# Performance work log

Measured on AMD Instinct MI355X. Metric: run time of the kernel, lower is better.

## Reference

```python
import jax, jax.numpy as jnp
import numpy as np

S, B, D, H, V = 1024, 4, 1024, 4096, 32000
EPS = 1e-5

def _ln(x, g, b):
    m = jnp.mean(x, axis=-1, keepdims=True)
    v = jnp.var(x, axis=-1, keepdims=True)
    return (x - m) * jax.lax.rsqrt(v + EPS) * g + b

def setup_inputs() -> dict:
    key = jax.random.key(0)
    ks = jax.random.split(key, 12)
    def xav(k, shape):
        fan_in, fan_out = shape[1], shape[0]
        lim = np.sqrt(6.0 / (fan_in + fan_out))
        return jax.random.uniform(k, shape, jnp.float32, -lim, lim)
    return {
        "inputs": jax.random.randint(ks[0], (S, B), 0, V, dtype=jnp.int32),
        "emb_table": jax.random.normal(ks[1], (V, D), jnp.float32),
        "WQ": xav(ks[2], (D, D)),
        "WK": xav(ks[3], (D, D)),
        "WV": xav(ks[4], (D, D)),
        "Wo": xav(ks[5], (D, D)),
        "bo": jnp.zeros((D,), jnp.float32),
        "W1": xav(ks[6], (H, D)),
        "b1": jnp.zeros((H,), jnp.float32),
        "W2": xav(ks[7], (D, H)),
        "b2": jnp.zeros((D,), jnp.float32),
        "g1": jnp.ones((D,), jnp.float32),
        "be1": jnp.zeros((D,), jnp.float32),
        "g2": jnp.ones((D,), jnp.float32),
        "be2": jnp.zeros((D,), jnp.float32),
        "Wd": xav(ks[8], (V, D)),
        "bd": jnp.zeros((V,), jnp.float32),
    }

def reference(inputs, emb_table, WQ, WK, WV, Wo, bo, W1, b1, W2, b2, g1, be1, g2, be2, Wd, bd):
    # inputs: [S, B] int ids
    emb = emb_table[inputs]                       # [S, B, D]
    # F.linear(x, W) == x @ W.T
    Q = jnp.einsum('sbd,ed->bse', emb, WQ)        # [B, S, D]
    K = jnp.einsum('sbd,ed->bse', emb, WK)
    Vv = jnp.einsum('sbd,ed->bse', emb, WV)
    scores = jnp.einsum('bqd,bkd->bqk', Q, K) / jnp.sqrt(jnp.float32(D))
    attn = jax.nn.softmax(scores, axis=-1)        # [B, S, S]
    z = jnp.einsum('bqk,bkd->qbd', attn, Vv)      # back to [S, B, D]
    z = jnp.einsum('sbd,ed->sbe', z, Wo) + bo
    x = _ln(emb + z, g1, be1)
    ffn = jnp.einsum('sbh,dh->sbd', jax.nn.relu(jnp.einsum('sbd,hd->sbh', x, W1) + b1), W2) + b2
    out = _ln(x + ffn, g2, be2)
    logits = out.reshape(S * B, D) @ Wd.T + bd    # [S*B, V]
    return logits
```

## Files before the change

kernel.cpp:

```cpp
#include <hip/hip_runtime.h>

typedef float f32x4 __attribute__((ext_vector_type(4)));
typedef __bf16 bf16x8 __attribute__((ext_vector_type(8)));
typedef int i32x4 __attribute__((ext_vector_type(4)));
typedef unsigned short u16;
typedef unsigned short u16x4 __attribute__((ext_vector_type(4)));
typedef unsigned short u16x8 __attribute__((ext_vector_type(8)));
typedef unsigned int u32;

#define SEQ 1024
#define NBATCH 4
#define DM 1024
#define HD 4096
#define NV 32000
#define NT (SEQ * NBATCH)

__device__ __forceinline__ u16 f2bf(float f) {
  u32 u = __builtin_bit_cast(u32, f);
  return (u16)((u + 0x7FFFu + ((u >> 16) & 1u)) >> 16);
}

__global__ __launch_bounds__(256) void cast_bf16_kernel(const float* __restrict__ in,
                                                        u16* __restrict__ out, int n8) {
  int i = blockIdx.x * 256 + threadIdx.x;
  if (i >= n8) return;
  const f32x4* p = (const f32x4*)(in + (long)i * 8);
  f32x4 a = p[0], b = p[1];
  u16x8 o;
  o[0] = f2bf(a[0]); o[1] = f2bf(a[1]); o[2] = f2bf(a[2]); o[3] = f2bf(a[3]);
  o[4] = f2bf(b[0]); o[5] = f2bf(b[1]); o[6] = f2bf(b[2]); o[7] = f2bf(b[3]);
  *(u16x8*)(out + (long)i * 8) = o;
}

__global__ __launch_bounds__(256) void embed_kernel(const int* __restrict__ ids,
                                                    const float* __restrict__ tab,
                                                    float* __restrict__ ef,
                                                    u16* __restrict__ eh) {
  int t = blockIdx.x, tid = threadIdx.x;
  long id = ids[t];
  f32x4 v = *(const f32x4*)(tab + id * DM + tid * 4);
  *(f32x4*)(ef + (long)t * DM + tid * 4) = v;
  u16x4 h;
  h[0] = f2bf(v[0]); h[1] = f2bf(v[1]); h[2] = f2bf(v[2]); h[3] = f2bf(v[3]);
  *(u16x4*)(eh + (long)t * DM + tid * 4) = h;
}

__global__ __launch_bounds__(256) void softmax_kernel(const float* __restrict__ s,
                                                      u16* __restrict__ p) {
  int row = blockIdx.x, tid = threadIdx.x;
  const float* rp = s + (long)row * SEQ;
  f32x4 v = *(const f32x4*)(rp + tid * 4);
  float mx = fmaxf(fmaxf(v[0], v[1]), fmaxf(v[2], v[3]));
  for (int o = 32; o; o >>= 1) mx = fmaxf(mx, __shfl_xor(mx, o));
  __shared__ float red[4];
  if ((tid & 63) == 0) red[tid >> 6] = mx;
  __syncthreads();
  mx = fmaxf(fmaxf(red[0], red[1]), fmaxf(red[2], red[3]));
  const float sc = 0.03125f;
  f32x4 e;
  e[0] = expf((v[0] - mx) * sc); e[1] = expf((v[1] - mx) * sc);
  e[2] = expf((v[2] - mx) * sc); e[3] = expf((v[3] - mx) * sc);
  float sm = e[0] + e[1] + e[2] + e[3];
  for (int o = 32; o; o >>= 1) sm += __shfl_xor(sm, o);
  __syncthreads();
  if ((tid & 63) == 0) red[tid >> 6] = sm;
  __syncthreads();
  sm = red[0] + red[1] + red[2] + red[3];
  float inv = 1.0f / sm;
  u16x4 o4;
  o4[0] = f2bf(e[0] * inv); o4[1] = f2bf(e[1] * inv);
  o4[2] = f2bf(e[2] * inv); o4[3] = f2bf(e[3] * inv);
  *(u16x4*)(p + (long)row * SEQ + tid * 4) = o4;
}

__global__ __launch_bounds__(256) void ln_kernel(const float* __restrict__ in,
                                                 const float* __restrict__ g,
                                                 const float* __restrict__ be,
                                                 float* __restrict__ outf,
                                                 u16* __restrict__ outh) {
  int row = blockIdx.x, tid = threadIdx.x;
  f32x4 v = *(const f32x4*)(in + (long)row * DM + tid * 4);
  float s = v[0] + v[1] + v[2] + v[3];
  float q = v[0] * v[0] + v[1] * v[1] + v[2] * v[2] + v[3] * v[3];
  for (int o = 32; o; o >>= 1) { s += __shfl_xor(s, o); q += __shfl_xor(q, o); }
  __shared__ float rs_[4], rq_[4];
  if ((tid & 63) == 0) { rs_[tid >> 6] = s; rq_[tid >> 6] = q; }
  __syncthreads();
  s = rs_[0] + rs_[1] + rs_[2] + rs_[3];
  q = rq_[0] + rq_[1] + rq_[2] + rq_[3];
  float mean = s * (1.0f / DM);
  float var = q * (1.0f / DM) - mean * mean;
  float rstd = rsqrtf(var + 1e-5f);
  f32x4 gg = *(const f32x4*)(g + tid * 4);
  f32x4 bb = *(const f32x4*)(be + tid * 4);
  f32x4 y;
  y[0] = (v[0] - mean) * rstd * gg[0] + bb[0];
  y[1] = (v[1] - mean) * rstd * gg[1] + bb[1];
  y[2] = (v[2] - mean) * rstd * gg[2] + bb[2];
  y[3] = (v[3] - mean) * rstd * gg[3] + bb[3];
  if (outf) *(f32x4*)(outf + (long)row * DM + tid * 4) = y;
  if (outh) {
    u16x4 h;
    h[0] = f2bf(y[0]); h[1] = f2bf(y[1]); h[2] = f2bf(y[2]); h[3] = f2bf(y[3]);
    *(u16x4*)(outh + (long)row * DM + tid * 4) = h;
  }
}

__global__ __launch_bounds__(256) void ln_i8_kernel(const float* __restrict__ in,
                                                    const float* __restrict__ g,
                                                    const float* __restrict__ be,
                                                    char* __restrict__ q8,
                                                    float* __restrict__ scale) {
  int row = blockIdx.x, tid = threadIdx.x;
  f32x4 v = *(const f32x4*)(in + (long)row * DM + tid * 4);
  float s = v[0] + v[1] + v[2] + v[3];
  float q = v[0] * v[0] + v[1] * v[1] + v[2] * v[2] + v[3] * v[3];
  for (int o = 32; o; o >>= 1) { s += __shfl_xor(s, o); q += __shfl_xor(q, o); }
  __shared__ float rs_[4], rq_[4], rm_[4];
  if ((tid & 63) == 0) { rs_[tid >> 6] = s; rq_[tid >> 6] = q; }
  __syncthreads();
  s = rs_[0] + rs_[1] + rs_[2] + rs_[3];
  q = rq_[0] + rq_[1] + rq_[2] + rq_[3];
  float mean = s * (1.0f / DM);
  float var = q * (1.0f / DM) - mean * mean;
  float rstd = rsqrtf(var + 1e-5f);
  f32x4 gg = *(const f32x4*)(g + tid * 4);
  f32x4 bb = *(const f32x4*)(be + tid * 4);
  f32x4 y;
  y[0] = (v[0] - mean) * rstd * gg[0] + bb[0];
  y[1] = (v[1] - mean) * rstd * gg[1] + bb[1];
  y[2] = (v[2] - mean) * rstd * gg[2] + bb[2];
  y[3] = (v[3] - mean) * rstd * gg[3] + bb[3];
  float am = fmaxf(fmaxf(fabsf(y[0]), fabsf(y[1])), fmaxf(fabsf(y[2]), fabsf(y[3])));
  for (int o = 32; o; o >>= 1) am = fmaxf(am, __shfl_xor(am, o));
  __syncthreads();
  if ((tid & 63) == 0) rm_[tid >> 6] = am;
  __syncthreads();
  am = fmaxf(fmaxf(rm_[0], rm_[1]), fmaxf(rm_[2], rm_[3]));
  float inv = (am > 0.f) ? 127.f / am : 0.f;
  int q0 = (int)rintf(y[0] * inv), q1 = (int)rintf(y[1] * inv);
  int q2 = (int)rintf(y[2] * inv), q3 = (int)rintf(y[3] * inv);
  u32 pk = (q0 & 255) | ((q1 & 255) << 8) | ((q2 & 255) << 16) | ((u32)(q3 & 255) << 24);
  *(u32*)(q8 + (size_t)row * DM + tid * 4) = pk;
  if (tid == 0) scale[row] = am * (1.0f / 127.f);
}

__global__ __launch_bounds__(256) void rowq_i8_kernel(const float* __restrict__ in,
                                                      char* __restrict__ q8,
                                                      float* __restrict__ scale) {
  int row = blockIdx.x, tid = threadIdx.x;
  f32x4 v = *(const f32x4*)(in + (size_t)row * DM + tid * 4);
  float am = fmaxf(fmaxf(fabsf(v[0]), fabsf(v[1])), fmaxf(fabsf(v[2]), fabsf(v[3])));
  for (int o = 32; o; o >>= 1) am = fmaxf(am, __shfl_xor(am, o));
  __shared__ float rm_[4];
  if ((tid & 63) == 0) rm_[tid >> 6] = am;
  __syncthreads();
  am = fmaxf(fmaxf(rm_[0], rm_[1]), fmaxf(rm_[2], rm_[3]));
  float inv = (am > 0.f) ? 127.f / am : 0.f;
  int q0 = (int)rintf(v[0] * inv), q1 = (int)rintf(v[1] * inv);
  int q2 = (int)rintf(v[2] * inv), q3 = (int)rintf(v[3] * inv);
  u32 pk = (q0 & 255) | ((q1 & 255) << 8) | ((q2 & 255) << 16) | ((u32)(q3 & 255) << 24);
  *(u32*)(q8 + (size_t)row * DM + tid * 4) = pk;
  if (tid == 0) scale[row] = am * (1.0f / 127.f);
}

#define GLD(gp, lp)                                              \
  __builtin_amdgcn_global_load_lds(                              \
      (__attribute__((address_space(1))) void*)(gp),             \
      (__attribute__((address_space(3))) void*)(lp), 16, 0, 0)

#define BM 128
#define BN 128
#define BK 32

__global__ __launch_bounds__(256) void gemm_bt(
    const u16* __restrict__ A, const u16* __restrict__ B,
    float* __restrict__ Cf, u16* __restrict__ Ch,
    const float* __restrict__ bias, const float* __restrict__ resid,
    int K, int lda, int ldb, int ldc,
    long batA, long batB, long batC, int relu) {
  __shared__ u16 As[BM * BK];
  __shared__ u16 Bs[BN * BK];
  const int tid = threadIdx.x;
  const int bz = blockIdx.z;
  A += (long)bz * batA;
  B += (long)bz * batB;
  const long cbase = (long)bz * batC;
  const int row0 = blockIdx.y * BM;
  const int col0 = blockIdx.x * BN;
  const int l = tid & 63;
  const int w = tid >> 6;
  const int wr = (w >> 1) * 64, wc = (w & 1) * 64;

  f32x4 acc[4][4] = {};

  const u16* gA = A + (long)(row0 + (tid >> 2)) * lda + (tid & 3) * 8;
  const u16* gB = B + (long)(col0 + (tid >> 2)) * ldb + (tid & 3) * 8;
  const long a64 = (long)64 * lda, b64 = (long)64 * ldb;
  u16* lA = As + tid * 8;
  u16* lB = Bs + tid * 8;

  const int fr = l & 15;
  const int fk = (l >> 4) * 8;
  const u16* rA = As + (wr + fr) * BK + fk;
  const u16* rB = Bs + (wc + fr) * BK + fk;

  for (int k0 = 0; k0 < K; k0 += BK) {
    GLD(gA + k0, lA);
    GLD(gA + a64 + k0, lA + 2048);
    GLD(gB + k0, lB);
    GLD(gB + b64 + k0, lB + 2048);
    __syncthreads();
    bf16x8 af[4], bf[4];
#pragma unroll
    for (int m = 0; m < 4; ++m) af[m] = *(const bf16x8*)(rA + m * 16 * BK);
#pragma unroll
    for (int n = 0; n < 4; ++n) bf[n] = *(const bf16x8*)(rB + n * 16 * BK);
#pragma unroll
    for (int m = 0; m < 4; ++m)
#pragma unroll
      for (int n = 0; n < 4; ++n)
        acc[m][n] = __builtin_amdgcn_mfma_f32_16x16x32_bf16(af[m], bf[n], acc[m][n], 0, 0, 0);
    __syncthreads();
  }

  const int er = row0 + wr + ((l >> 4) << 2);
  const int ec = col0 + wc + (l & 15);
#pragma unroll
  for (int m = 0; m < 4; ++m) {
#pragma unroll
    for (int n = 0; n < 4; ++n) {
      f32x4 v = acc[m][n];
      const int c = ec + n * 16;
      float bv = bias ? bias[c] : 0.0f;
#pragma unroll
      for (int i = 0; i < 4; ++i) {
        const int r = er + m * 16 + i;
        float x = v[i] + bv;
        if (resid) x += resid[(long)r * ldc + c];
        if (relu) x = fmaxf(x, 0.0f);
        if (Cf) Cf[cbase + (long)r * ldc + c] = x;
        if (Ch) Ch[cbase + (long)r * ldc + c] = f2bf(x);
      }
    }
  }
}

#define DSB() __builtin_amdgcn_sched_barrier(0)
#define SBAR() __builtin_amdgcn_s_barrier()

__global__ __launch_bounds__(256) void gemm_i8(
    const char* __restrict__ A, const char* __restrict__ B,
    float* __restrict__ C, const float* __restrict__ sA, const float* __restrict__ sB,
    const float* __restrict__ bias, int K, int lda, int ldb, int ldc,
    int Mtiles, int Ntiles) {
  __shared__ __align__(16) char As[3][128 * 64];
  __shared__ __align__(16) char Bs[3][128 * 64];
  const int tid = threadIdx.x;

  const int nwg = gridDim.x;
  const int blk = blockIdx.x;
  const int cpx = nwg >> 3;
  const int wg = (blk & 7) * cpx + (blk >> 3);
  const int gsz = 4 * Ntiles;
  const int gid = wg / gsz;
  const int rem = wg - gid * gsz;
  const int row0 = (gid * 4 + (rem & 3)) * 128;
  const int col0 = (rem >> 2) * 128;

  const int l = tid & 63;
  const int w = tid >> 6;
  const int wr = (w >> 1) * 64, wc = (w & 1) * 64;

  const int srow = tid >> 2;
  const int sslot = (tid & 3) ^ ((srow >> 1) & 3);
  const char* gA = A + (size_t)(row0 + srow) * lda + sslot * 16;
  const char* gB = B + (size_t)(col0 + srow) * ldb + sslot * 16;
  const size_t a64 = (size_t)64 * lda, b64 = (size_t)64 * ldb;

#define STAGE_I8(buf, kt)                                            \
  do {                                                               \
    const char* _ga = gA + (size_t)(kt) * 64;                        \
    const char* _gb = gB + (size_t)(kt) * 64;                        \
    GLD(_ga, &As[buf][0] + tid * 16);                                \
    GLD(_ga + a64, &As[buf][4096] + tid * 16);                       \
    GLD(_gb, &Bs[buf][0] + tid * 16);                                \
    GLD(_gb + b64, &Bs[buf][4096] + tid * 16);                       \
  } while (0)

  const int fr = l & 15;
  const int fsw = 16 * ((l >> 4) ^ ((fr >> 1) & 3));
  const int raoff = (wr + fr) * 64 + fsw;
  const int rboff = (wc + fr) * 64 + fsw;

  i32x4 acc[4][4] = {};

#define COMPUTE_I8(buf)                                                         \
  do {                                                                          \
    i32x4 af[4], bf[4];                                                         \
    _Pragma("unroll")                                                           \
    for (int m = 0; m < 4; ++m) af[m] = *(const i32x4*)(&As[buf][raoff + m * 1024]); \
    _Pragma("unroll")                                                           \
    for (int n = 0; n < 4; ++n) bf[n] = *(const i32x4*)(&Bs[buf][rboff + n * 1024]); \
    _Pragma("unroll")                                                           \
    for (int m = 0; m < 4; ++m)                                                 \
      _Pragma("unroll")                                                         \
      for (int n = 0; n < 4; ++n)                                               \
        acc[m][n] = __builtin_amdgcn_mfma_i32_16x16x64_i8(af[m], bf[n], acc[m][n], 0, 0, 0); \
  } while (0)

  const int nkt = K >> 6;

  STAGE_I8(0, 0);
  STAGE_I8(1, 1);
  asm volatile("s_waitcnt vmcnt(4)"); DSB();
  SBAR();

  for (int t = 0; t < nkt - 2; ++t) {
    const int b2 = (t + 2) % 3;
    STAGE_I8(b2, t + 2);
    COMPUTE_I8(t % 3);
    asm volatile("s_waitcnt vmcnt(4)"); DSB();
    SBAR();
  }
  COMPUTE_I8((nkt - 2) % 3);
  asm volatile("s_waitcnt vmcnt(0)"); DSB();
  SBAR();
  COMPUTE_I8((nkt - 1) % 3);

  const int er = row0 + wr + ((l >> 4) << 2);
  const int ec = col0 + wc + (l & 15);
#pragma unroll
  for (int m = 0; m < 4; ++m) {
#pragma unroll
    for (int n = 0; n < 4; ++n) {
      i32x4 v = acc[m][n];
      const int c = ec + n * 16;
      const float sb = sB[c];
      const float bv = bias ? bias[c] : 0.0f;
#pragma unroll
      for (int i = 0; i < 4; ++i) {
        const int r = er + m * 16 + i;
        C[(size_t)r * ldc + c] = (float)v[i] * (sA[r] * sb) + bv;
      }
    }
  }
#undef STAGE_I8
#undef COMPUTE_I8
}

template <int N0, int N1>
__device__ __forceinline__ void mfma16(f32x4 (&acc)[8][4], const bf16x8 (&af)[8],
                                       bf16x8 b0, bf16x8 b1) {
#pragma unroll
  for (int m = 0; m < 8; ++m) {
    acc[m][N0] = __builtin_amdgcn_mfma_f32_16x16x32_bf16(af[m], b0, acc[m][N0], 0, 0, 0);
    acc[m][N1] = __builtin_amdgcn_mfma_f32_16x16x32_bf16(af[m], b1, acc[m][N1], 0, 0, 0);
  }
}

__global__ __launch_bounds__(512, 2) void gemm256_bt(
    const u16* __restrict__ A, const u16* __restrict__ B,
    float* __restrict__ Cf, u16* __restrict__ Ch,
    const float* __restrict__ bias,
    int K, int lda, int ldb, int ldc, int Mtiles, int Ntiles, int relu) {
  __shared__ __align__(16) u16 As[2][2][128 * 64];
  __shared__ __align__(16) u16 Bs[2][2][256 * 32];
  const int tid = threadIdx.x;

  const int nwg = gridDim.x;
  const int blk = blockIdx.x;
  const int cpx = nwg >> 3;
  const int wg = (blk & 7) * cpx + (blk >> 3);
  const int gsz = 4 * Ntiles;
  const int gid = wg / gsz;
  const int rem = wg - gid * gsz;
  const int row0 = (gid * 4 + (rem & 3)) * 256;
  const int col0 = (rem >> 2) * 256;

  const int l = tid & 63;
  const int w = tid >> 6;
  const int wr = w >> 2;
  const int wc = w & 3;

  const int sArow = tid >> 3;
  const int sAcol = ((tid & 7) ^ ((sArow >> 1) & 7)) * 8;
  const int sBrow = tid >> 2;
  const int sBcol = ((tid & 3) ^ ((sBrow >> 2) & 3)) * 8;

  const u16* gA = A + (size_t)(row0 + sArow) * lda + sAcol;
  const u16* gB = B + (size_t)(col0 + sBrow) * ldb + sBcol;
  const size_t a64 = (size_t)64 * lda;
  const size_t b128 = (size_t)128 * ldb;

#define STAGE_A(buf, h, kt)                                          \
  do {                                                               \
    const u16* _g = gA + (size_t)(h) * 128 * lda + (size_t)(kt) * 64;\
    u16* _l = &As[buf][h][0] + tid * 8;                              \
    GLD(_g, _l);                                                     \
    GLD(_g + a64, _l + 4096);                                        \
  } while (0)
#define STAGE_B(buf, kk, kt)                                         \
  do {                                                               \
    const u16* _g = gB + (size_t)(kt) * 64 + (kk) * 32;              \
    u16* _l = &Bs[buf][kk][0] + tid * 8;                             \
    GLD(_g, _l);                                                     \
    GLD(_g + b128, _l + 4096);                                       \
  } while (0)

  const int fr = l & 15;
  const int g8 = (l >> 4) * 8;
  const int acp0 = g8 ^ (((fr >> 1) & 7) * 8);
  const int acp1 = (32 + g8) ^ (((fr >> 1) & 7) * 8);
  const int bcp = g8 ^ (((fr >> 2) & 3) * 8);

#define RA(buf, m, cp) (*(const bf16x8*)(&As[buf][wr][((m) * 16 + fr) * 64 + (cp)]))
#define RB(buf, n, kk) (*(const bf16x8*)(&Bs[buf][kk][(wc * 64 + (n) * 16 + fr) * 32 + bcp]))

  f32x4 acc[8][4] = {};
  bf16x8 a0[8], a1[8], bb0, bb1;

  const int nkt = K >> 6;
  const int nit = nkt >> 1;

  STAGE_A(0, 0, 0); STAGE_A(0, 1, 0);
  STAGE_B(0, 0, 0); STAGE_B(0, 1, 0);
  STAGE_B(1, 0, 1); STAGE_A(1, 0, 1);
  asm volatile("s_waitcnt vmcnt(4)"); DSB();
  SBAR();

  for (int i = 0; i < nit; ++i) {
    const int u = 2 * i + 1;
    const int v = (2 * i + 2 < nkt) ? 2 * i + 2 : nkt - 1;
    const int w2 = (2 * i + 3 < nkt) ? 2 * i + 3 : nkt - 1;

#pragma unroll
    for (int m = 0; m < 8; ++m) a0[m] = RA(0, m, acp0);
    bb0 = RB(0, 0, 0); bb1 = RB(0, 1, 0);
    STAGE_A(1, 1, u);
    SBAR();
    asm volatile("s_waitcnt lgkmcnt(0)"); DSB();
    __builtin_amdgcn_s_setprio(1);
    mfma16<0, 1>(acc, a0, bb0, bb1);
    __builtin_amdgcn_s_setprio(0);
    SBAR();
    bb0 = RB(0, 2, 0); bb1 = RB(0, 3, 0);
    STAGE_B(1, 1, u);
    asm volatile("s_waitcnt vmcnt(6)"); DSB();
    SBAR();
    asm volatile("s_waitcnt lgkmcnt(0)"); DSB();
    __builtin_amdgcn_s_setprio(1);
    mfma16<2, 3>(acc, a0, bb0, bb1);
    __builtin_amdgcn_s_setprio(0);
    SBAR();
#pragma unroll
    for (int m = 0; m < 8; ++m) a1[m] = RA(0, m, acp1);
    bb0 = RB(0, 0, 1); bb1 = RB(0, 1, 1);
    STAGE_B(0, 0, v);
    SBAR();
    asm volatile("s_waitcnt lgkmcnt(0)"); DSB();
    __builtin_amdgcn_s_setprio(1);
    mfma16<0, 1>(acc, a1, bb0, bb1);
    __builtin_amdgcn_s_setprio(0);
    SBAR();
    bb0 = RB(0, 2, 1); bb1 = RB(0, 3, 1);
    STAGE_A(0, 0, v);
    asm volatile("s_waitcnt vmcnt(6)"); DSB();
    SBAR();
    asm volatile("s_waitcnt lgkmcnt(0)"); DSB();
    __builtin_amdgcn_s_setprio(1);
    mfma16<2, 3>(acc, a1, bb0, bb1);
    __builtin_amdgcn_s_setprio(0);
    SBAR();
#pragma unroll
    for (int m = 0; m < 8; ++m) a0[m] = RA(1, m, acp0);
    bb0 = RB(1, 0, 0); bb1 = RB(1, 1, 0);
    STAGE_A(0, 1, v);
    SBAR();
    asm volatile("s_waitcnt lgkmcnt(0)"); DSB();
    __builtin_amdgcn_s_setprio(1);
    mfma16<0, 1>(acc, a0, bb0, bb1);
    __builtin_amdgcn_s_setprio(0);
    SBAR();
    bb0 = RB(1, 2, 0); bb1 = RB(1, 3, 0);
    STAGE_B(0, 1, v);
    asm volatile("s_waitcnt vmcnt(6)"); DSB();
    SBAR();
    asm volatile("s_waitcnt lgkmcnt(0)"); DSB();
    __builtin_amdgcn_s_setprio(1);
    mfma16<2, 3>(acc, a0, bb0, bb1);
    __builtin_amdgcn_s_setprio(0);
    SBAR();
#pragma unroll
    for (int m = 0; m < 8; ++m) a1[m] = RA(1, m, acp1);
    bb0 = RB(1, 0, 1); bb1 = RB(1, 1, 1);
    STAGE_B(1, 0, w2);
    SBAR();
    asm volatile("s_waitcnt lgkmcnt(0)"); DSB();
    __builtin_amdgcn_s_setprio(1);
    mfma16<0, 1>(acc, a1, bb0, bb1);
    __builtin_amdgcn_s_setprio(0);
    SBAR();
    bb0 = RB(1, 2, 1); bb1 = RB(1, 3, 1);
    STAGE_A(1, 0, w2);
    asm volatile("s_waitcnt vmcnt(6)"); DSB();
    SBAR();
    asm volatile("s_waitcnt lgkmcnt(0)"); DSB();
    __builtin_amdgcn_s_setprio(1);
    mfma16<2, 3>(acc, a1, bb0, bb1);
    __builtin_amdgcn_s_setprio(0);
    SBAR();
  }

  asm volatile("s_waitcnt vmcnt(0)"); DSB();

  const int er = row0 + wr * 128 + ((l >> 4) << 2);
  const int ec = col0 + wc * 64 + (l & 15);
#pragma unroll
  for (int m = 0; m < 8; ++m) {
#pragma unroll
    for (int n = 0; n < 4; ++n) {
      f32x4 vv = acc[m][n];
      const int c = ec + n * 16;
      float bv = bias ? bias[c] : 0.0f;
#pragma unroll
      for (int i = 0; i < 4; ++i) {
        const int r = er + m * 16 + i;
        float x = vv[i] + bv;
        if (relu) x = fmaxf(x, 0.0f);
        if (Cf) Cf[(size_t)r * ldc + c] = x;
        if (Ch) Ch[(size_t)r * ldc + c] = f2bf(x);
      }
    }
  }
#undef STAGE_A
#undef STAGE_B
#undef RA
#undef RB
}

extern "C" void kernel_launch(void* const* d_in, const int* in_sizes, int n_in,
                              void* d_out, int out_size, void* d_ws, size_t ws_size,
                              hipStream_t stream) {
  const int* ids = (const int*)d_in[0];
  const float* tab = (const float*)d_in[1];
  const float* WQ = (const float*)d_in[2];
  const float* WK = (const float*)d_in[3];
  const float* WV = (const float*)d_in[4];
  const float* Wo = (const float*)d_in[5];
  const float* bo = (const float*)d_in[6];
  const float* W1 = (const float*)d_in[7];
  const float* b1 = (const float*)d_in[8];
  const float* W2 = (const float*)d_in[9];
  const float* b2 = (const float*)d_in[10];
  const float* g1 = (const float*)d_in[11];
  const float* be1 = (const float*)d_in[12];
  const float* g2 = (const float*)d_in[13];
  const float* be2 = (const float*)d_in[14];
  const float* Wd = (const float*)d_in[15];
  const float* bd = (const float*)d_in[16];
  float* logits = (float*)d_out;

  if (ws_size < 280000000ull) return;

  char* p = (char*)d_ws;
  auto alloc = [&](size_t bytes) {
    char* r = p;
    p += (bytes + 255) & ~(size_t)255;
    return r;
  };
  float* embf = (float*)alloc((size_t)NT * DM * 4);
  u16* embh = (u16*)alloc((size_t)NT * DM * 2);
  u16* WQKh = (u16*)alloc((size_t)2 * DM * DM * 2);
  u16* WVh = (u16*)alloc((size_t)DM * DM * 2);
  u16* Woh = (u16*)alloc((size_t)DM * DM * 2);
  u16* W1h = (u16*)alloc((size_t)HD * DM * 2);
  u16* W2h = (u16*)alloc((size_t)DM * HD * 2);
  char* Wdq = (char*)alloc((size_t)NV * DM);
  float* sWd = (float*)alloc((size_t)NV * 4);
  u16* QKh = (u16*)alloc((size_t)NT * 2 * DM * 2);
  u16* VTh = (u16*)alloc((size_t)NBATCH * DM * SEQ * 2);
  float* scoresf = (float*)alloc((size_t)NBATCH * SEQ * SEQ * 4);
  u16* Ph = (u16*)alloc((size_t)NBATCH * SEQ * SEQ * 2);
  u16* zh = (u16*)alloc((size_t)NT * DM * 2);
  float* r1f = (float*)alloc((size_t)NT * DM * 4);
  float* xf = (float*)alloc((size_t)NT * DM * 4);
  u16* xh = (u16*)alloc((size_t)NT * DM * 2);
  u16* hh = (u16*)alloc((size_t)NT * HD * 2);
  float* r2f = (float*)alloc((size_t)NT * DM * 4);
  char* outq = (char*)alloc((size_t)NT * DM);
  float* sOut = (float*)alloc((size_t)NT * 4);

  cast_bf16_kernel<<<dim3(DM * DM / 8 / 256), 256, 0, stream>>>(WQ, WQKh, DM * DM / 8);
  cast_bf16_kernel<<<dim3(DM * DM / 8 / 256), 256, 0, stream>>>(WK, WQKh + (size_t)DM * DM, DM * DM / 8);
  cast_bf16_kernel<<<dim3(DM * DM / 8 / 256), 256, 0, stream>>>(WV, WVh, DM * DM / 8);
  cast_bf16_kernel<<<dim3(DM * DM / 8 / 256), 256, 0, stream>>>(Wo, Woh, DM * DM / 8);
  cast_bf16_kernel<<<dim3(HD * DM / 8 / 256), 256, 0, stream>>>(W1, W1h, HD * DM / 8);
  cast_bf16_kernel<<<dim3(DM * HD / 8 / 256), 256, 0, stream>>>(W2, W2h, DM * HD / 8);
  rowq_i8_kernel<<<dim3(NV), 256, 0, stream>>>(Wd, Wdq, sWd);

  embed_kernel<<<NT, 256, 0, stream>>>(ids, tab, embf, embh);

  gemm_bt<<<dim3(2 * DM / BN, NT / BM, 1), 256, 0, stream>>>(
      embh, WQKh, nullptr, QKh, nullptr, nullptr, DM, DM, DM, 2 * DM, 0, 0, 0, 0);

  gemm_bt<<<dim3(SEQ / BN, DM / BM, NBATCH), 256, 0, stream>>>(
      WVh, embh, nullptr, VTh, nullptr, nullptr, DM, DM, NBATCH * DM, SEQ,
      0, DM, (long)DM * SEQ, 0);

  gemm_bt<<<dim3(SEQ / BN, SEQ / BM, NBATCH), 256, 0, stream>>>(
      QKh, QKh + DM, scoresf, nullptr, nullptr, nullptr, DM,
      NBATCH * 2 * DM, NBATCH * 2 * DM, SEQ,
      2 * DM, 2 * DM, (long)SEQ * SEQ, 0);

  softmax_kernel<<<NBATCH * SEQ, 256, 0, stream>>>(scoresf, Ph);

  gemm_bt<<<dim3(DM / BN, SEQ / BM, NBATCH), 256, 0, stream>>>(
      Ph, VTh, nullptr, zh, nullptr, nullptr, SEQ, SEQ, SEQ, NBATCH * DM,
      (long)SEQ * SEQ, (long)DM * SEQ, DM, 0);

  gemm_bt<<<dim3(DM / BN, NT / BM, 1), 256, 0, stream>>>(
      zh, Woh, r1f, nullptr, bo, embf, DM, DM, DM, DM, 0, 0, 0, 0);

  ln_kernel<<<NT, 256, 0, stream>>>(r1f, g1, be1, xf, xh);

  gemm256_bt<<<dim3((NT / 256) * (HD / 256)), 512, 0, stream>>>(
      xh, W1h, nullptr, hh, b1, DM, DM, DM, HD, NT / 256, HD / 256, 1);
  gemm_bt<<<dim3(DM / BN, NT / BM, 1), 256, 0, stream>>>(
      hh, W2h, r2f, nullptr, b2, xf, HD, HD, HD, DM, 0, 0, 0, 0);

  ln_i8_kernel<<<NT, 256, 0, stream>>>(r2f, g2, be2, outq, sOut);

  gemm_i8<<<dim3((NT / 128) * (NV / 128)), 256, 0, stream>>>(
      outq, Wdq, logits, sOut, sWd, bd, DM, DM, DM, NV, NT / 128, NV / 128);
}
```

Before: 769.5 us.

## Merge weight casts into one launch, simplify int8 GEMM tile mapping, unroll pipeline

```diff
diff --git a/kernel.cpp b/kernel.cpp
--- a/kernel.cpp
+++ b/kernel.cpp
@@ -20,16 +20,34 @@
   return (u16)((u + 0x7FFFu + ((u >> 16) & 1u)) >> 16);
 }
 
-__global__ __launch_bounds__(256) void cast_bf16_kernel(const float* __restrict__ in,
-                                                        u16* __restrict__ out, int n8) {
-  int i = blockIdx.x * 256 + threadIdx.x;
-  if (i >= n8) return;
-  const f32x4* p = (const f32x4*)(in + (long)i * 8);
+__global__ __launch_bounds__(256) void cast_all_kernel(
+    const float* __restrict__ wq, const float* __restrict__ wk,
+    const float* __restrict__ wv, const float* __restrict__ wo,
+    const float* __restrict__ w1, const float* __restrict__ w2,
+    u16* __restrict__ wqk, u16* __restrict__ wvh, u16* __restrict__ woh,
+    u16* __restrict__ w1h, u16* __restrict__ w2h) {
+  long i = (long)blockIdx.x * 256 + threadIdx.x;
+  const float* src;
+  u16* dst;
+  long off;
+  if (i < 262144) {
+    if (i < 131072) { src = wq; off = i; } else { src = wk; off = i - 131072; }
+    dst = wqk + i * 8;
+  } else if (i < 393216) {
+    src = wv; off = i - 262144; dst = wvh + off * 8;
+  } else if (i < 524288) {
+    src = wo; off = i - 393216; dst = woh + off * 8;
+  } else if (i < 1048576) {
+    src = w1; off = i - 524288; dst = w1h + off * 8;
+  } else {
+    src = w2; off = i - 1048576; dst = w2h + off * 8;
+  }
+  const f32x4* p = (const f32x4*)(src + off * 8);
   f32x4 a = p[0], b = p[1];
   u16x8 o;
   o[0] = f2bf(a[0]); o[1] = f2bf(a[1]); o[2] = f2bf(a[2]); o[3] = f2bf(a[3]);
   o[4] = f2bf(b[0]); o[5] = f2bf(b[1]); o[6] = f2bf(b[2]); o[7] = f2bf(b[3]);
-  *(u16x8*)(out + (long)i * 8) = o;
+  *(u16x8*)dst = o;
 }
 
 __global__ __launch_bounds__(256) void embed_kernel(const int* __restrict__ ids,
@@ -262,11 +280,8 @@
   const int blk = blockIdx.x;
   const int cpx = nwg >> 3;
   const int wg = (blk & 7) * cpx + (blk >> 3);
-  const int gsz = 4 * Ntiles;
-  const int gid = wg / gsz;
-  const int rem = wg - gid * gsz;
-  const int row0 = (gid * 4 + (rem & 3)) * 128;
-  const int col0 = (rem >> 2) * 128;
+  const int row0 = (wg / Ntiles) * 128;
+  const int col0 = (wg % Ntiles) * 128;
 
   const int l = tid & 63;
   const int w = tid >> 6;
@@ -309,6 +324,14 @@
         acc[m][n] = __builtin_amdgcn_mfma_i32_16x16x64_i8(af[m], bf[n], acc[m][n], 0, 0, 0); \
   } while (0)
 
+#define PIPE_STEP(bufS, kt, bufC)                    \
+  do {                                               \
+    STAGE_I8(bufS, kt);                              \
+    COMPUTE_I8(bufC);                                \
+    asm volatile("s_waitcnt vmcnt(4)"); DSB();       \
+    SBAR();                                          \
+  } while (0)
+
   const int nkt = K >> 6;
 
   STAGE_I8(0, 0);
@@ -316,17 +339,17 @@
   asm volatile("s_waitcnt vmcnt(4)"); DSB();
   SBAR();
 
-  for (int t = 0; t < nkt - 2; ++t) {
-    const int b2 = (t + 2) % 3;
-    STAGE_I8(b2, t + 2);
-    COMPUTE_I8(t % 3);
-    asm volatile("s_waitcnt vmcnt(4)"); DSB();
-    SBAR();
-  }
-  COMPUTE_I8((nkt - 2) % 3);
+  for (int t = 0; t + 7 <= nkt; t += 3) {
+    PIPE_STEP(2, t + 2, 0);
+    PIPE_STEP(0, t + 3, 1);
+    PIPE_STEP(1, t + 4, 2);
+  }
+  PIPE_STEP(2, 14, 0);
+  PIPE_STEP(0, 15, 1);
+  COMPUTE_I8(2);
   asm volatile("s_waitcnt vmcnt(0)"); DSB();
   SBAR();
-  COMPUTE_I8((nkt - 1) % 3);
+  COMPUTE_I8(0);
 
   const int er = row0 + wr + ((l >> 4) << 2);
   const int ec = col0 + wc + (l & 15);
@@ -347,6 +370,7 @@
   }
 #undef STAGE_I8
 #undef COMPUTE_I8
+#undef PIPE_STEP
 }
 
 template <int N0, int N1>
@@ -591,12 +615,8 @@
   char* outq = (char*)alloc((size_t)NT * DM);
   float* sOut = (float*)alloc((size_t)NT * 4);
 
-  cast_bf16_kernel<<<dim3(DM * DM / 8 / 256), 256, 0, stream>>>(WQ, WQKh, DM * DM / 8);
-  cast_bf16_kernel<<<dim3(DM * DM / 8 / 256), 256, 0, stream>>>(WK, WQKh + (size_t)DM * DM, DM * DM / 8);
-  cast_bf16_kernel<<<dim3(DM * DM / 8 / 256), 256, 0, stream>>>(WV, WVh, DM * DM / 8);
-  cast_bf16_kernel<<<dim3(DM * DM / 8 / 256), 256, 0, stream>>>(Wo, Woh, DM * DM / 8);
-  cast_bf16_kernel<<<dim3(HD * DM / 8 / 256), 256, 0, stream>>>(W1, W1h, HD * DM / 8);
-  cast_bf16_kernel<<<dim3(DM * HD / 8 / 256), 256, 0, stream>>>(W2, W2h, DM * HD / 8);
+  cast_all_kernel<<<dim3(6144), 256, 0, stream>>>(WQ, WK, WV, Wo, W1, W2,
+                                                  WQKh, WVh, Woh, W1h, W2h);
   rowq_i8_kernel<<<dim3(NV), 256, 0, stream>>>(Wd, Wdq, sWd);
 
   embed_kernel<<<NT, 256, 0, stream>>>(ids, tab, embf, embh);
```

New measurement: 712.1 us. 1.08x faster.
